# Kernel optimization log

Hardware: AMD Instinct MI355X
Metric: run time of the kernel (lower is better)

The kernel has to match this reference:

```python
import jax, jax.numpy as jnp
import numpy as np

BLOCK = 64
CRIT_TH = 0.5
NEGL_TH = 0.01
TEMP = 1.0
EPS = 1e-6


def setup_inputs() -> dict:
    key = jax.random.key(0)
    kq, kk, kv = jax.random.split(key, 3)
    B, T, H, D = 1, 2048, 8, 64
    q = jax.random.normal(kq, (B, T, H, D), dtype=jnp.float32)
    k = jax.random.normal(kk, (B, T, H, D), dtype=jnp.float32)
    v = jax.random.normal(kv, (B, T, H, D), dtype=jnp.float32)
    return {"q": q, "k": k, "v": v}


def _classify_blocks(qb, kb, D):
    # qb: [B,nq,bs,H,D], kb: [B,nk,bs,H,D]
    q_rep = qb.mean(axis=2)  # [B,nq,H,D]
    k_rep = kb.mean(axis=2)  # [B,nk,H,D]
    bscores = jnp.einsum('bqhd,bkhd->bhqk', q_rep, k_rep) / np.float32(np.sqrt(D))
    ssm = jax.nn.softmax(bscores, axis=-1)
    var = jnp.var(ssm, axis=-1, ddof=1, keepdims=True)  # unbiased, matches torch .var()
    max_scores = bscores.max(axis=-1, keepdims=True)
    imp = var * jnp.maximum(max_scores - bscores.min(), EPS)
    imp_n = (imp - imp.min()) / (imp.max() - imp.min() + EPS)
    crit = imp_n >= CRIT_TH
    negl = imp_n <= NEGL_TH
    marg = (~crit) & (~negl)
    return crit, marg


def reference(q, k, v):
    B, T, H, D = q.shape
    S = k.shape[1]
    nq, nk = T // BLOCK, S // BLOCK  # T,S are multiples of BLOCK (no padding needed)
    dtype = q.dtype

    qb = q.reshape(B, nq, BLOCK, H, D)
    kb = k.reshape(B, nk, BLOCK, H, D)
    vb = v.reshape(B, nk, BLOCK, H, D)

    crit, marg = _classify_blocks(qb, kb, D)  # [B,H,nq,nk] bool
    critf = crit.astype(dtype)
    margf = marg.astype(dtype)

    # ---- exact (critical) blocks: per-block-pair softmax attention ----
    scale = np.float32(1.0 / (np.sqrt(D) * TEMP))
    scores = jnp.einsum('bqthd,bkshd->bhqkts', qb, kb) * scale  # [B,H,nq,nk,bs,bs]
    attn = jax.nn.softmax(scores.astype(jnp.float32), axis=-1).astype(dtype)
    attn_m = attn * critf[:, :, :, :, None, None]
    out_c = jnp.einsum('bhqkts,bkshd->bqthd', attn_m, vb)  # [B,nq,bs,H,D]
    w_c = jnp.einsum('bhqkts->bqth', attn_m)[..., None]    # [B,nq,bs,H,1]

    # ---- linear (marginal) blocks: ELU+1 feature-map attention ----
    qf = jax.nn.elu(qb / TEMP) + 1.0
    kf = jax.nn.elu(kb / TEMP) + 1.0
    kv = jnp.einsum('bkshd,bkshv->bkhdv', kf, vb)              # [B,nk,H,D,D]
    num = jnp.einsum('bqthd,bkhdv->bqkthv', qf, kv)            # [B,nq,nk,bs,H,D]
    k_sum = kf.sum(axis=2)                                     # [B,nk,H,D]
    den = jnp.einsum('bqthd,bkhd->bqkth', qf, k_sum) + EPS     # [B,nq,nk,bs,H]
    out_pair = num / den[..., None]
    out_l = jnp.einsum('bqkthd,bhqk->bqthd', out_pair, margf)
    w_l = jnp.einsum('bqkth,bhqk->bqth', den, margf)[..., None]

    out = (out_c + out_l) / (w_c + w_l + EPS)
    return out.reshape(B, T, H, D)
```

## Files before the change

kernel.cpp:

```cpp
#include <hip/hip_runtime.h>
#include <math.h>

namespace {
constexpr int H  = 8;
constexpr int D  = 64;
constexpr int NB = 32;
constexpr int BS = 64;
constexpr int QST = 68;
}
#define FEPS 1e-6f

typedef unsigned short u16;
typedef unsigned int   u32;
typedef __attribute__((ext_vector_type(8))) short bf16x8;
typedef __attribute__((ext_vector_type(4))) float floatx4;

__device__ __forceinline__ u32 f2bf(float x) {
  union { float f; u32 u; } v; v.f = x;
  return (v.u + 0x7FFFu + ((v.u >> 16) & 1u)) >> 16;
}
__device__ __forceinline__ u32 pk2(float a, float b) { return f2bf(a) | (f2bf(b) << 16); }
#define ELU1(x) ((x) > 0.f ? (x) + 1.f : expf(x))
#define SWZ(row, kblk) ((row)*64 + (((kblk) ^ ((row)&7))*8))

__global__ __launch_bounds__(256) void prep_kernel(const float* __restrict__ q,
                                                   const float* __restrict__ k,
                                                   const float* __restrict__ v,
                                                   float* __restrict__ kvt,
                                                   float* __restrict__ ksum,
                                                   double* __restrict__ qrep,
                                                   double* __restrict__ krep) {
  __shared__ float smem[3*BS*D];
  int bid = blockIdx.x;
  int tid = threadIdx.x;
  if (bid >= 256) {
    double* qred = (double*)smem;
    int r = bid - 256;
    int h = r >> 5, bi = r & 31;
    int d = tid & 63, quarter = tid >> 6;
    double s = 0.0;
    for (int t = quarter*16; t < quarter*16 + 16; ++t)
      s += (double)q[((bi*BS + t)*H + h)*D + d];
    qred[quarter*64 + d] = s;
    __syncthreads();
    if (tid < 64)
      qrep[r*D + tid] = (qred[tid] + qred[64+tid] + qred[128+tid] + qred[192+tid]) * (1.0/64.0);
    return;
  }
  float* kf   = smem;
  float* vv   = smem + BS*D;
  float* kraw = smem + 2*BS*D;
  int h = bid >> 5, ki = bid & 31;
  int sr = tid >> 2, cg = tid & 3;
  const float4* kb = (const float4*)(k + ((ki*BS + sr)*H + h)*D);
  const float4* vb = (const float4*)(v + ((ki*BS + sr)*H + h)*D);
#pragma unroll
  for (int m = 0; m < 4; ++m) {
    float4 kk = kb[cg*4 + m];
    float4 vx = vb[cg*4 + m];
    int c = cg*16 + m*4;
    *(float4*)&kraw[sr*D + c] = kk;
    kf[sr*D + c + 0] = ELU1(kk.x);
    kf[sr*D + c + 1] = ELU1(kk.y);
    kf[sr*D + c + 2] = ELU1(kk.z);
    kf[sr*D + c + 3] = ELU1(kk.w);
    *(float4*)&vv[sr*D + c] = vx;
  }
  __syncthreads();
  int c = tid & 63, dg = tid >> 6, d0 = dg*16;
  float acc[16];
#pragma unroll
  for (int j = 0; j < 16; ++j) acc[j] = 0.f;
#pragma unroll 4
  for (int s2 = 0; s2 < BS; ++s2) {
    float vval = vv[s2*D + c];
    const float4* kr = (const float4*)&kf[s2*D + d0];
    float4 a0 = kr[0], a1 = kr[1], a2 = kr[2], a3 = kr[3];
    acc[0]  += vval*a0.x; acc[1]  += vval*a0.y; acc[2]  += vval*a0.z; acc[3]  += vval*a0.w;
    acc[4]  += vval*a1.x; acc[5]  += vval*a1.y; acc[6]  += vval*a1.z; acc[7]  += vval*a1.w;
    acc[8]  += vval*a2.x; acc[9]  += vval*a2.y; acc[10] += vval*a2.z; acc[11] += vval*a2.w;
    acc[12] += vval*a3.x; acc[13] += vval*a3.y; acc[14] += vval*a3.z; acc[15] += vval*a3.w;
  }
  float* op = kvt + (size_t)bid*4096 + c*64 + d0;
  *(float4*)(op + 0)  = make_float4(acc[0],  acc[1],  acc[2],  acc[3]);
  *(float4*)(op + 4)  = make_float4(acc[4],  acc[5],  acc[6],  acc[7]);
  *(float4*)(op + 8)  = make_float4(acc[8],  acc[9],  acc[10], acc[11]);
  *(float4*)(op + 12) = make_float4(acc[12], acc[13], acc[14], acc[15]);
  if (dg == 0) {
    float ks = 0.f;
    for (int s2 = 0; s2 < BS; ++s2) ks += kf[s2*D + c];
    ksum[bid*D + c] = ks;
    double m = 0.0;
    for (int s2 = 0; s2 < BS; ++s2) m += (double)kraw[s2*D + c];
    krep[bid*D + c] = m * (1.0/64.0);
  }
}

__global__ __launch_bounds__(256) void bscore_kernel(const double* __restrict__ qrep,
                                                     const double* __restrict__ krep,
                                                     double* __restrict__ bsc) {
  int tid = threadIdx.x;
  int lr = tid >> 5, ki = tid & 31;
  int r = blockIdx.x * 8 + lr;
  int h = r >> 5;
  const double* qr = qrep + r*D;
  const double* kr = krep + (h*NB + ki)*D;
  double s = 0.0;
#pragma unroll 16
  for (int d = 0; d < D; ++d) s += qr[d]*kr[d];
  bsc[r*NB + ki] = s * 0.125;
}

__global__ __launch_bounds__(256) void classify2_kernel(const double* __restrict__ bsc,
                                                        int* __restrict__ flags) {
  __shared__ double red[256];
  int tid = threadIdx.x;
  const double* row = bsc + tid*NB;
  double rmax = -1.0e300, rmin = 1.0e300;
#pragma unroll 8
  for (int i = 0; i < NB; ++i) { double b = row[i]; rmax = fmax(rmax, b); rmin = fmin(rmin, b); }
  red[tid] = rmin; __syncthreads();
  for (int s = 128; s > 0; s >>= 1) { if (tid < s) red[tid] = fmin(red[tid], red[tid+s]); __syncthreads(); }
  double gmin = red[0]; __syncthreads();
  double S = 0.0;
#pragma unroll 8
  for (int i = 0; i < NB; ++i) S += exp(row[i] - rmax);
  double invS = 1.0 / S;
  double psum = 0.0;
#pragma unroll 8
  for (int i = 0; i < NB; ++i) psum += exp(row[i] - rmax) * invS;
  double mu = psum * (1.0/32.0);
  double var = 0.0;
#pragma unroll 8
  for (int i = 0; i < NB; ++i) {
    double dv = exp(row[i] - rmax) * invS - mu;
    var += dv*dv;
  }
  var *= (1.0/31.0);
  double rng = rmax - gmin;
  if (rng < 1e-6) rng = 1e-6;
  double imp = var * rng;
  red[tid] = imp; __syncthreads();
  for (int s = 128; s > 0; s >>= 1) { if (tid < s) red[tid] = fmin(red[tid], red[tid+s]); __syncthreads(); }
  double imin = red[0]; __syncthreads();
  red[tid] = imp; __syncthreads();
  for (int s = 128; s > 0; s >>= 1) { if (tid < s) red[tid] = fmax(red[tid], red[tid+s]); __syncthreads(); }
  double imax = red[0];
  double impn = (imp - imin) / (imax - imin + 1e-6);
  flags[tid] = (impn >= 0.5) ? 2 : ((impn <= 0.01) ? 0 : 1);
}

__global__ __launch_bounds__(256) void main_kernel(
    const float* __restrict__ q, const float* __restrict__ k, const float* __restrict__ v,
    const float* __restrict__ kvt, const float* __restrict__ ksum,
    const int* __restrict__ flags,
    float* __restrict__ pacc, float* __restrict__ pwsum,
    float* __restrict__ outDirect, int kn) {
  __shared__ float smem[8768];
  int bid = blockIdx.x & 255;
  int chunk = blockIdx.x >> 8;
  int k0 = chunk * kn;
  int h = bid >> 5, qi = bid & 31;
  int tid = threadIdx.x;
  int row = tid >> 2, cg = tid & 3, c0 = cg*16;
  int lane = tid & 63;
  int flag = flags[bid];

  if (flag == 1) {
    u16*  qfb  = (u16*)smem;
    u16*  kvb  = (u16*)(smem + 2048);
    float* idens = smem + 4096;
    float* wsl   = smem + 6144;
    float* kslc  = smem + 6208;

    {
      const float4* kss = (const float4*)(ksum + (size_t)(h*NB + k0)*D);
      for (int i = tid; i < kn*16; i += 256) ((float4*)kslc)[i] = kss[i];
    }
    float qf[16];
    {
      const float4* qp = (const float4*)(q + ((qi*BS + row)*H + h)*D + c0);
      float4 q0 = qp[0], q1 = qp[1], q2 = qp[2], q3 = qp[3];
      qf[0]=ELU1(q0.x); qf[1]=ELU1(q0.y); qf[2]=ELU1(q0.z); qf[3]=ELU1(q0.w);
      qf[4]=ELU1(q1.x); qf[5]=ELU1(q1.y); qf[6]=ELU1(q1.z); qf[7]=ELU1(q1.w);
      qf[8]=ELU1(q2.x); qf[9]=ELU1(q2.y); qf[10]=ELU1(q2.z); qf[11]=ELU1(q2.w);
      qf[12]=ELU1(q3.x); qf[13]=ELU1(q3.y); qf[14]=ELU1(q3.z); qf[15]=ELU1(q3.w);
      uint4 p0, p1;
      p0.x = pk2(qf[0],qf[1]);  p0.y = pk2(qf[2],qf[3]);
      p0.z = pk2(qf[4],qf[5]);  p0.w = pk2(qf[6],qf[7]);
      p1.x = pk2(qf[8],qf[9]);  p1.y = pk2(qf[10],qf[11]);
      p1.z = pk2(qf[12],qf[13]); p1.w = pk2(qf[14],qf[15]);
      *(uint4*)&qfb[SWZ(row, cg*2)]     = p0;
      *(uint4*)&qfb[SWZ(row, cg*2 + 1)] = p1;
    }
    __syncthreads();
    {
      float wloc = 0.f;
      for (int ki = 0; ki < kn; ++ki) {
        float pd = 0.f;
#pragma unroll
        for (int j = 0; j < 16; ++j) pd += qf[j] * kslc[ki*64 + c0 + j];
        pd += __shfl_xor(pd, 1, 64);
        pd += __shfl_xor(pd, 2, 64);
        float den = pd + FEPS;
        if (cg == 0) idens[row*32 + ki] = 1.0f / den;
        wloc += den;
      }
      if (cg == 0) wsl[row] = wloc;
    }
    __syncthreads();
    int w = tid >> 6, m = lane & 15, quad = lane >> 4;
    bf16x8 aLo = *(const bf16x8*)&qfb[SWZ(w*16 + m, quad)];
    bf16x8 aHi = *(const bf16x8*)&qfb[SWZ(w*16 + m, 4 + quad)];
    const bf16x8* bLo[4]; const bf16x8* bHi[4];
#pragma unroll
    for (int t = 0; t < 4; ++t) {
      bLo[t] = (const bf16x8*)&kvb[SWZ(t*16 + m, quad)];
      bHi[t] = (const bf16x8*)&kvb[SWZ(t*16 + m, 4 + quad)];
    }
    int rbase = w*16 + quad*4;
    float acc[16];
#pragma unroll
    for (int j = 0; j < 16; ++j) acc[j] = 0.f;

    for (int ki = 0; ki < kn; ++ki) {
      const float4* kvp = (const float4*)(kvt + (size_t)(h*NB + k0 + ki)*4096 + row*64 + c0);
      float4 a0 = kvp[0], a1 = kvp[1], a2 = kvp[2], a3 = kvp[3];
      uint4 p0, p1;
      p0.x = pk2(a0.x,a0.y); p0.y = pk2(a0.z,a0.w);
      p0.z = pk2(a1.x,a1.y); p0.w = pk2(a1.z,a1.w);
      p1.x = pk2(a2.x,a2.y); p1.y = pk2(a2.z,a2.w);
      p1.z = pk2(a3.x,a3.y); p1.w = pk2(a3.z,a3.w);
      *(uint4*)&kvb[SWZ(row, cg*2)]     = p0;
      *(uint4*)&kvb[SWZ(row, cg*2 + 1)] = p1;
      __syncthreads();
      float i0 = idens[(rbase + 0)*32 + ki];
      float i1 = idens[(rbase + 1)*32 + ki];
      float i2 = idens[(rbase + 2)*32 + ki];
      float i3 = idens[(rbase + 3)*32 + ki];
      floatx4 zz = {0.f, 0.f, 0.f, 0.f};
#pragma unroll
      for (int t = 0; t < 4; ++t) {
        floatx4 c4 = __builtin_amdgcn_mfma_f32_16x16x32_bf16(aLo, *bLo[t], zz, 0, 0, 0);
        c4 = __builtin_amdgcn_mfma_f32_16x16x32_bf16(aHi, *bHi[t], c4, 0, 0, 0);
        acc[t*4+0] += c4[0]*i0;
        acc[t*4+1] += c4[1]*i1;
        acc[t*4+2] += c4[2]*i2;
        acc[t*4+3] += c4[3]*i3;
      }
      __syncthreads();
    }
    if (outDirect) {
#pragma unroll
      for (int r = 0; r < 4; ++r) {
        float wd = 1.0f / (wsl[rbase + r] + FEPS);
        float* op = outDirect + ((qi*BS + rbase + r)*H + h)*D + m;
#pragma unroll
        for (int t = 0; t < 4; ++t) op[t*16] = acc[t*4+r]*wd;
      }
    } else {
#pragma unroll
      for (int r = 0; r < 4; ++r) {
        float* pa = pacc + ((size_t)blockIdx.x*64 + rbase + r)*64 + m;
#pragma unroll
        for (int t = 0; t < 4; ++t) pa[t*16] = acc[t*4+r];
      }
      if (tid < 64) pwsum[(size_t)blockIdx.x*64 + tid] = wsl[tid];
    }
    return;
  }

  float* bufA = smem;
  float* bufB = smem + 4352;
  float acc[16];
#pragma unroll
  for (int j = 0; j < 16; ++j) acc[j] = 0.f;
  float wsum = 0.f;

  if (flag == 2) {
    const float4* qp = (const float4*)(q + ((qi*BS + row)*H + h)*D);
#pragma unroll
    for (int mm = 0; mm < 4; ++mm) {
      float4 qq = qp[cg*4 + mm];
      int c = c0 + mm*4;
      bufA[row*QST + c + 0] = qq.x*0.125f;
      bufA[row*QST + c + 1] = qq.y*0.125f;
      bufA[row*QST + c + 2] = qq.z*0.125f;
      bufA[row*QST + c + 3] = qq.w*0.125f;
    }
    __syncthreads();
    for (int ki = k0; ki < k0 + kn; ++ki) {
      const float4* kp = (const float4*)(k + ((ki*BS + row)*H + h)*D);
#pragma unroll
      for (int mm = 0; mm < 4; ++mm)
        *(float4*)&bufB[row*QST + c0 + mm*4] = kp[cg*4 + mm];
      __syncthreads();
      float sc[16];
#pragma unroll
      for (int j = 0; j < 16; ++j) sc[j] = 0.f;
      for (int d = 0; d < D; ++d) {
        float a = bufA[row*QST + d];
#pragma unroll
        for (int j = 0; j < 16; ++j)
          sc[j] += a * bufB[(c0 + j)*QST + d];
      }
      float mx = sc[0];
#pragma unroll
      for (int j = 1; j < 16; ++j) mx = fmaxf(mx, sc[j]);
      mx = fmaxf(mx, __shfl_xor(mx, 1, 64));
      mx = fmaxf(mx, __shfl_xor(mx, 2, 64));
      float es = 0.f;
      float p[16];
#pragma unroll
      for (int j = 0; j < 16; ++j) { p[j] = expf(sc[j] - mx); es += p[j]; }
      es += __shfl_xor(es, 1, 64);
      es += __shfl_xor(es, 2, 64);
      float inv = 1.0f / es;
#pragma unroll
      for (int j = 0; j < 16; ++j) p[j] *= inv;
      wsum += es * inv;
      __syncthreads();
      const float4* vp = (const float4*)(v + ((ki*BS + row)*H + h)*D);
#pragma unroll
      for (int mm = 0; mm < 4; ++mm)
        *(float4*)&bufB[row*QST + c0 + mm*4] = vp[cg*4 + mm];
      __syncthreads();
      for (int s2 = 0; s2 < BS; ++s2) {
        int g = s2 >> 4, jj = s2 & 15;
        float pv = __shfl(p[jj], (lane & ~3) | g, 64);
        const float4* vr = (const float4*)&bufB[s2*QST + c0];
        float4 a0 = vr[0], a1 = vr[1], a2 = vr[2], a3 = vr[3];
        acc[0]  += pv*a0.x; acc[1]  += pv*a0.y; acc[2]  += pv*a0.z; acc[3]  += pv*a0.w;
        acc[4]  += pv*a1.x; acc[5]  += pv*a1.y; acc[6]  += pv*a1.z; acc[7]  += pv*a1.w;
        acc[8]  += pv*a2.x; acc[9]  += pv*a2.y; acc[10] += pv*a2.z; acc[11] += pv*a2.w;
        acc[12] += pv*a3.x; acc[13] += pv*a3.y; acc[14] += pv*a3.z; acc[15] += pv*a3.w;
      }
      __syncthreads();
    }
  }
  if (outDirect) {
    float wd = 1.0f / (wsum + FEPS);
    float* op = outDirect + ((qi*BS + row)*H + h)*D + c0;
    *(float4*)(op + 0)  = make_float4(acc[0]*wd,  acc[1]*wd,  acc[2]*wd,  acc[3]*wd);
    *(float4*)(op + 4)  = make_float4(acc[4]*wd,  acc[5]*wd,  acc[6]*wd,  acc[7]*wd);
    *(float4*)(op + 8)  = make_float4(acc[8]*wd,  acc[9]*wd,  acc[10]*wd, acc[11]*wd);
    *(float4*)(op + 12) = make_float4(acc[12]*wd, acc[13]*wd, acc[14]*wd, acc[15]*wd);
  } else {
    float* pa = pacc + ((size_t)blockIdx.x*64 + row)*64 + c0;
    *(float4*)(pa + 0)  = make_float4(acc[0],  acc[1],  acc[2],  acc[3]);
    *(float4*)(pa + 4)  = make_float4(acc[4],  acc[5],  acc[6],  acc[7]);
    *(float4*)(pa + 8)  = make_float4(acc[8],  acc[9],  acc[10], acc[11]);
    *(float4*)(pa + 12) = make_float4(acc[12], acc[13], acc[14], acc[15]);
    if (cg == 0) pwsum[(size_t)blockIdx.x*64 + row] = wsum;
  }
}

__global__ __launch_bounds__(256) void reduce_kernel(const float* __restrict__ pacc,
                                                     const float* __restrict__ pwsum,
                                                     float* __restrict__ out, int ksplit) {
  int bid = blockIdx.x;
  int h = bid >> 5, qi = bid & 31;
  int tid = threadIdx.x;
  int row = tid >> 2, c0 = (tid & 3)*16;
  float acc[16];
#pragma unroll
  for (int j = 0; j < 16; ++j) acc[j] = 0.f;
  float ws = 0.f;
  for (int s = 0; s < ksplit; ++s) {
    const float* pa = pacc + ((size_t)(s*256 + bid)*64 + row)*64 + c0;
    float4 a0 = ((const float4*)pa)[0], a1 = ((const float4*)pa)[1];
    float4 a2 = ((const float4*)pa)[2], a3 = ((const float4*)pa)[3];
    acc[0]  += a0.x; acc[1]  += a0.y; acc[2]  += a0.z; acc[3]  += a0.w;
    acc[4]  += a1.x; acc[5]  += a1.y; acc[6]  += a1.z; acc[7]  += a1.w;
    acc[8]  += a2.x; acc[9]  += a2.y; acc[10] += a2.z; acc[11] += a2.w;
    acc[12] += a3.x; acc[13] += a3.y; acc[14] += a3.z; acc[15] += a3.w;
    ws += pwsum[(size_t)(s*256 + bid)*64 + row];
  }
  float wd = 1.0f / (ws + FEPS);
  float* op = out + ((qi*BS + row)*H + h)*D + c0;
  *(float4*)(op + 0)  = make_float4(acc[0]*wd,  acc[1]*wd,  acc[2]*wd,  acc[3]*wd);
  *(float4*)(op + 4)  = make_float4(acc[4]*wd,  acc[5]*wd,  acc[6]*wd,  acc[7]*wd);
  *(float4*)(op + 8)  = make_float4(acc[8]*wd,  acc[9]*wd,  acc[10]*wd, acc[11]*wd);
  *(float4*)(op + 12) = make_float4(acc[12]*wd, acc[13]*wd, acc[14]*wd, acc[15]*wd);
}

extern "C" void kernel_launch(void* const* d_in, const int* in_sizes, int n_in,
                              void* d_out, int out_size, void* d_ws, size_t ws_size,
                              hipStream_t stream) {
  const float* q = (const float*)d_in[0];
  const float* k = (const float*)d_in[1];
  const float* v = (const float*)d_in[2];
  float* out = (float*)d_out;
  char* ws = (char*)d_ws;
  double* qrep = (double*)(ws + 0);
  double* krep = (double*)(ws + 131072);
  int*    flg  = (int*)   (ws + 262144);
  float*  ksw  = (float*) (ws + 263168);
  float*  kvw  = (float*) (ws + 328704);
  double* bsc  = (double*)(ws + 4523008);
  float*  pws  = (float*) (ws + 4588544);
  float*  pac  = (float*) (ws + 4850688);

  size_t base = 4850688;
  int ksplit = (ws_size >= base + 4ull*4194304) ? 4
             : (ws_size >= base + 2ull*4194304) ? 2
             : (ws_size >= base + 1ull*4194304) ? 1 : 0;

  prep_kernel<<<512, 256, 0, stream>>>(q, k, v, kvw, ksw, qrep, krep);
  bscore_kernel<<<32, 256, 0, stream>>>(qrep, krep, bsc);
  classify2_kernel<<<1, 256, 0, stream>>>(bsc, flg);
  if (ksplit >= 1) {
    main_kernel<<<ksplit*256, 256, 0, stream>>>(q, k, v, kvw, ksw, flg,
                                                pac, pws, nullptr, NB/ksplit);
    reduce_kernel<<<256, 256, 0, stream>>>(pac, pws, out, ksplit);
  } else {
    main_kernel<<<256, 256, 0, stream>>>(q, k, v, kvw, ksw, flg,
                                         nullptr, nullptr, out, NB);
  }
}
```

Baseline: 120.7 us.

## Drop k-split and reduce kernel, double-buffer KV tiles, single-pass variance

```diff
diff --git a/kernel.cpp b/kernel.cpp
--- a/kernel.cpp
+++ b/kernel.cpp
@@ -111,7 +111,7 @@
   bsc[r*NB + ki] = s * 0.125;
 }
 
-__global__ __launch_bounds__(256) void classify2_kernel(const double* __restrict__ bsc,
+__global__ __launch_bounds__(256) void classify3_kernel(const double* __restrict__ bsc,
                                                         int* __restrict__ flags) {
   __shared__ double red[256];
   int tid = threadIdx.x;
@@ -122,21 +122,13 @@
   red[tid] = rmin; __syncthreads();
   for (int s = 128; s > 0; s >>= 1) { if (tid < s) red[tid] = fmin(red[tid], red[tid+s]); __syncthreads(); }
   double gmin = red[0]; __syncthreads();
-  double S = 0.0;
+  double S = 0.0, S2 = 0.0;
 #pragma unroll 8
-  for (int i = 0; i < NB; ++i) S += exp(row[i] - rmax);
+  for (int i = 0; i < NB; ++i) { double e = exp(row[i] - rmax); S += e; S2 += e*e; }
   double invS = 1.0 / S;
-  double psum = 0.0;
-#pragma unroll 8
-  for (int i = 0; i < NB; ++i) psum += exp(row[i] - rmax) * invS;
-  double mu = psum * (1.0/32.0);
-  double var = 0.0;
-#pragma unroll 8
-  for (int i = 0; i < NB; ++i) {
-    double dv = exp(row[i] - rmax) * invS - mu;
-    var += dv*dv;
-  }
-  var *= (1.0/31.0);
+  double sp = S * invS;
+  double mu = sp * (1.0/32.0);
+  double var = (S2*invS*invS - 2.0*mu*sp + 32.0*mu*mu) * (1.0/31.0);
   double rng = rmax - gmin;
   if (rng < 1e-6) rng = 1e-6;
   double imp = var * rng;
@@ -153,13 +145,9 @@
 __global__ __launch_bounds__(256) void main_kernel(
     const float* __restrict__ q, const float* __restrict__ k, const float* __restrict__ v,
     const float* __restrict__ kvt, const float* __restrict__ ksum,
-    const int* __restrict__ flags,
-    float* __restrict__ pacc, float* __restrict__ pwsum,
-    float* __restrict__ outDirect, int kn) {
-  __shared__ float smem[8768];
-  int bid = blockIdx.x & 255;
-  int chunk = blockIdx.x >> 8;
-  int k0 = chunk * kn;
+    const int* __restrict__ flags, float* __restrict__ out) {
+  __shared__ float smem[10304];
+  int bid = blockIdx.x;
   int h = bid >> 5, qi = bid & 31;
   int tid = threadIdx.x;
   int row = tid >> 2, cg = tid & 3, c0 = cg*16;
@@ -169,13 +157,13 @@
   if (flag == 1) {
     u16*  qfb  = (u16*)smem;
     u16*  kvb  = (u16*)(smem + 2048);
-    float* idens = smem + 4096;
-    float* wsl   = smem + 6144;
-    float* kslc  = smem + 6208;
-
-    {
-      const float4* kss = (const float4*)(ksum + (size_t)(h*NB + k0)*D);
-      for (int i = tid; i < kn*16; i += 256) ((float4*)kslc)[i] = kss[i];
+    float* idens = smem + 6144;
+    float* wsl   = smem + 8192;
+    float* kslc  = smem + 8256;
+
+    {
+      const float4* kss = (const float4*)(ksum + (size_t)(h*NB)*D);
+      for (int i = tid; i < NB*16; i += 256) ((float4*)kslc)[i] = kss[i];
     }
     float qf[16];
     {
@@ -193,10 +181,16 @@
       *(uint4*)&qfb[SWZ(row, cg*2)]     = p0;
       *(uint4*)&qfb[SWZ(row, cg*2 + 1)] = p1;
     }
+    const float* kvbase = kvt + (size_t)(h*NB)*4096 + row*64 + c0;
+    float4 t0, t1, t2, t3;
+    {
+      const float4* kvp = (const float4*)kvbase;
+      t0 = kvp[0]; t1 = kvp[1]; t2 = kvp[2]; t3 = kvp[3];
+    }
     __syncthreads();
     {
       float wloc = 0.f;
-      for (int ki = 0; ki < kn; ++ki) {
+      for (int ki = 0; ki < NB; ++ki) {
         float pd = 0.f;
 #pragma unroll
         for (int j = 0; j < 16; ++j) pd += qf[j] * kslc[ki*64 + c0 + j];
@@ -208,32 +202,30 @@
       }
       if (cg == 0) wsl[row] = wloc;
     }
-    __syncthreads();
+    {
+      uint4 p0, p1;
+      p0.x = pk2(t0.x,t0.y); p0.y = pk2(t0.z,t0.w);
+      p0.z = pk2(t1.x,t1.y); p0.w = pk2(t1.z,t1.w);
+      p1.x = pk2(t2.x,t2.y); p1.y = pk2(t2.z,t2.w);
+      p1.z = pk2(t3.x,t3.y); p1.w = pk2(t3.z,t3.w);
+      *(uint4*)&kvb[SWZ(row, cg*2)]     = p0;
+      *(uint4*)&kvb[SWZ(row, cg*2 + 1)] = p1;
+    }
     int w = tid >> 6, m = lane & 15, quad = lane >> 4;
     bf16x8 aLo = *(const bf16x8*)&qfb[SWZ(w*16 + m, quad)];
     bf16x8 aHi = *(const bf16x8*)&qfb[SWZ(w*16 + m, 4 + quad)];
-    const bf16x8* bLo[4]; const bf16x8* bHi[4];
-#pragma unroll
-    for (int t = 0; t < 4; ++t) {
-      bLo[t] = (const bf16x8*)&kvb[SWZ(t*16 + m, quad)];
-      bHi[t] = (const bf16x8*)&kvb[SWZ(t*16 + m, 4 + quad)];
-    }
     int rbase = w*16 + quad*4;
     float acc[16];
 #pragma unroll
     for (int j = 0; j < 16; ++j) acc[j] = 0.f;
 
-    for (int ki = 0; ki < kn; ++ki) {
-      const float4* kvp = (const float4*)(kvt + (size_t)(h*NB + k0 + ki)*4096 + row*64 + c0);
-      float4 a0 = kvp[0], a1 = kvp[1], a2 = kvp[2], a3 = kvp[3];
-      uint4 p0, p1;
-      p0.x = pk2(a0.x,a0.y); p0.y = pk2(a0.z,a0.w);
-      p0.z = pk2(a1.x,a1.y); p0.w = pk2(a1.z,a1.w);
-      p1.x = pk2(a2.x,a2.y); p1.y = pk2(a2.z,a2.w);
-      p1.z = pk2(a3.x,a3.y); p1.w = pk2(a3.z,a3.w);
-      *(uint4*)&kvb[SWZ(row, cg*2)]     = p0;
-      *(uint4*)&kvb[SWZ(row, cg*2 + 1)] = p1;
-      __syncthreads();
+    for (int ki = 0; ki < NB; ++ki) {
+      if (ki + 1 < NB) {
+        const float4* kvp = (const float4*)(kvbase + (size_t)(ki+1)*4096);
+        t0 = kvp[0]; t1 = kvp[1]; t2 = kvp[2]; t3 = kvp[3];
+      }
+      __syncthreads();
+      const u16* kb = kvb + (ki & 1)*4096;
       float i0 = idens[(rbase + 0)*32 + ki];
       float i1 = idens[(rbase + 1)*32 + ki];
       float i2 = idens[(rbase + 2)*32 + ki];
@@ -241,31 +233,32 @@
       floatx4 zz = {0.f, 0.f, 0.f, 0.f};
 #pragma unroll
       for (int t = 0; t < 4; ++t) {
-        floatx4 c4 = __builtin_amdgcn_mfma_f32_16x16x32_bf16(aLo, *bLo[t], zz, 0, 0, 0);
-        c4 = __builtin_amdgcn_mfma_f32_16x16x32_bf16(aHi, *bHi[t], c4, 0, 0, 0);
+        bf16x8 bLo = *(const bf16x8*)&kb[SWZ(t*16 + m, quad)];
+        bf16x8 bHi = *(const bf16x8*)&kb[SWZ(t*16 + m, 4 + quad)];
+        floatx4 c4 = __builtin_amdgcn_mfma_f32_16x16x32_bf16(aLo, bLo, zz, 0, 0, 0);
+        c4 = __builtin_amdgcn_mfma_f32_16x16x32_bf16(aHi, bHi, c4, 0, 0, 0);
         acc[t*4+0] += c4[0]*i0;
         acc[t*4+1] += c4[1]*i1;
         acc[t*4+2] += c4[2]*i2;
         acc[t*4+3] += c4[3]*i3;
       }
-      __syncthreads();
-    }
-    if (outDirect) {
-#pragma unroll
-      for (int r = 0; r < 4; ++r) {
-        float wd = 1.0f / (wsl[rbase + r] + FEPS);
-        float* op = outDirect + ((qi*BS + rbase + r)*H + h)*D + m;
-#pragma unroll
-        for (int t = 0; t < 4; ++t) op[t*16] = acc[t*4+r]*wd;
-      }
-    } else {
-#pragma unroll
-      for (int r = 0; r < 4; ++r) {
-        float* pa = pacc + ((size_t)blockIdx.x*64 + rbase + r)*64 + m;
-#pragma unroll
-        for (int t = 0; t < 4; ++t) pa[t*16] = acc[t*4+r];
-      }
-      if (tid < 64) pwsum[(size_t)blockIdx.x*64 + tid] = wsl[tid];
+      if (ki + 1 < NB) {
+        u16* kw = kvb + ((ki+1) & 1)*4096;
+        uint4 p0, p1;
+        p0.x = pk2(t0.x,t0.y); p0.y = pk2(t0.z,t0.w);
+        p0.z = pk2(t1.x,t1.y); p0.w = pk2(t1.z,t1.w);
+        p1.x = pk2(t2.x,t2.y); p1.y = pk2(t2.z,t2.w);
+        p1.z = pk2(t3.x,t3.y); p1.w = pk2(t3.z,t3.w);
+        *(uint4*)&kw[SWZ(row, cg*2)]     = p0;
+        *(uint4*)&kw[SWZ(row, cg*2 + 1)] = p1;
+      }
+    }
+#pragma unroll
+    for (int r = 0; r < 4; ++r) {
+      float wd = 1.0f / (wsl[rbase + r] + FEPS);
+      float* op = out + ((qi*BS + rbase + r)*H + h)*D + m;
+#pragma unroll
+      for (int t = 0; t < 4; ++t) op[t*16] = acc[t*4+r]*wd;
     }
     return;
   }
@@ -289,7 +282,7 @@
       bufA[row*QST + c + 3] = qq.w*0.125f;
     }
     __syncthreads();
-    for (int ki = k0; ki < k0 + kn; ++ki) {
+    for (int ki = 0; ki < NB; ++ki) {
       const float4* kp = (const float4*)(k + ((ki*BS + row)*H + h)*D);
 #pragma unroll
       for (int mm = 0; mm < 4; ++mm)
@@ -338,45 +331,7 @@
       __syncthreads();
     }
   }
-  if (outDirect) {
-    float wd = 1.0f / (wsum + FEPS);
-    float* op = outDirect + ((qi*BS + row)*H + h)*D + c0;
-    *(float4*)(op + 0)  = make_float4(acc[0]*wd,  acc[1]*wd,  acc[2]*wd,  acc[3]*wd);
-    *(float4*)(op + 4)  = make_float4(acc[4]*wd,  acc[5]*wd,  acc[6]*wd,  acc[7]*wd);
-    *(float4*)(op + 8)  = make_float4(acc[8]*wd,  acc[9]*wd,  acc[10]*wd, acc[11]*wd);
-    *(float4*)(op + 12) = make_float4(acc[12]*wd, acc[13]*wd, acc[14]*wd, acc[15]*wd);
-  } else {
-    float* pa = pacc + ((size_t)blockIdx.x*64 + row)*64 + c0;
-    *(float4*)(pa + 0)  = make_float4(acc[0],  acc[1],  acc[2],  acc[3]);
-    *(float4*)(pa + 4)  = make_float4(acc[4],  acc[5],  acc[6],  acc[7]);
-    *(float4*)(pa + 8)  = make_float4(acc[8],  acc[9],  acc[10], acc[11]);
-    *(float4*)(pa + 12) = make_float4(acc[12], acc[13], acc[14], acc[15]);
-    if (cg == 0) pwsum[(size_t)blockIdx.x*64 + row] = wsum;
-  }
-}
-
-__global__ __launch_bounds__(256) void reduce_kernel(const float* __restrict__ pacc,
-                                                     const float* __restrict__ pwsum,
-                                                     float* __restrict__ out, int ksplit) {
-  int bid = blockIdx.x;
-  int h = bid >> 5, qi = bid & 31;
-  int tid = threadIdx.x;
-  int row = tid >> 2, c0 = (tid & 3)*16;
-  float acc[16];
-#pragma unroll
-  for (int j = 0; j < 16; ++j) acc[j] = 0.f;
-  float ws = 0.f;
-  for (int s = 0; s < ksplit; ++s) {
-    const float* pa = pacc + ((size_t)(s*256 + bid)*64 + row)*64 + c0;
-    float4 a0 = ((const float4*)pa)[0], a1 = ((const float4*)pa)[1];
-    float4 a2 = ((const float4*)pa)[2], a3 = ((const float4*)pa)[3];
-    acc[0]  += a0.x; acc[1]  += a0.y; acc[2]  += a0.z; acc[3]  += a0.w;
-    acc[4]  += a1.x; acc[5]  += a1.y; acc[6]  += a1.z; acc[7]  += a1.w;
-    acc[8]  += a2.x; acc[9]  += a2.y; acc[10] += a2.z; acc[11] += a2.w;
-    acc[12] += a3.x; acc[13] += a3.y; acc[14] += a3.z; acc[15] += a3.w;
-    ws += pwsum[(size_t)(s*256 + bid)*64 + row];
-  }
-  float wd = 1.0f / (ws + FEPS);
+  float wd = 1.0f / (wsum + FEPS);
   float* op = out + ((qi*BS + row)*H + h)*D + c0;
   *(float4*)(op + 0)  = make_float4(acc[0]*wd,  acc[1]*wd,  acc[2]*wd,  acc[3]*wd);
   *(float4*)(op + 4)  = make_float4(acc[4]*wd,  acc[5]*wd,  acc[6]*wd,  acc[7]*wd);
@@ -398,23 +353,9 @@
   float*  ksw  = (float*) (ws + 263168);
   float*  kvw  = (float*) (ws + 328704);
   double* bsc  = (double*)(ws + 4523008);
-  float*  pws  = (float*) (ws + 4588544);
-  float*  pac  = (float*) (ws + 4850688);
-
-  size_t base = 4850688;
-  int ksplit = (ws_size >= base + 4ull*4194304) ? 4
-             : (ws_size >= base + 2ull*4194304) ? 2
-             : (ws_size >= base + 1ull*4194304) ? 1 : 0;
 
   prep_kernel<<<512, 256, 0, stream>>>(q, k, v, kvw, ksw, qrep, krep);
   bscore_kernel<<<32, 256, 0, stream>>>(qrep, krep, bsc);
-  classify2_kernel<<<1, 256, 0, stream>>>(bsc, flg);
-  if (ksplit >= 1) {
-    main_kernel<<<ksplit*256, 256, 0, stream>>>(q, k, v, kvw, ksw, flg,
-                                                pac, pws, nullptr, NB/ksplit);
-    reduce_kernel<<<256, 256, 0, stream>>>(pac, pws, out, ksplit);
-  } else {
-    main_kernel<<<256, 256, 0, stream>>>(q, k, v, kvw, ksw, flg,
-                                         nullptr, nullptr, out, NB);
-  }
-}
+  classify3_kernel<<<1, 256, 0, stream>>>(bsc, flg);
+  main_kernel<<<256, 256, 0, stream>>>(q, k, v, kvw, ksw, flg, out);
+}
```

Result: faster. 109.7 us (-9.1%).
